# Kernel optimization log

Measured on AMD Instinct MI355X. Metric: run time of the kernel, lower is better.

Reference implementation:

```python
import jax, jax.numpy as jnp
import numpy as np

N_CLASSES = 9
N_GROUPS = 2


def setup_inputs() -> dict:
    key = jax.random.key(0)
    k1, k2 = jax.random.split(key)
    N = 16_777_216  # number of samples
    preds = jax.random.randint(k1, (N,), 0, N_CLASSES, dtype=jnp.int32)
    attrs = jax.random.randint(k2, (N,), 0, N_GROUPS, dtype=jnp.int32)
    return {"preds": preds, "attrs": attrs}


def reference(preds, attrs):
    # Fused histogram: flatten (class, group) -> single bin id in [0, 18)
    flat = preds * N_GROUPS + attrs  # [N]
    counts = jax.ops.segment_sum(
        jnp.ones_like(flat, dtype=jnp.float32), flat,
        num_segments=N_CLASSES * N_GROUPS,
    ).reshape(N_CLASSES, N_GROUPS)  # [9, 2] histogram

    n_attr_1 = jnp.sum(attrs != 0).astype(jnp.float32)
    n_attr_0 = jnp.float32(attrs.shape[0]) - n_attr_1

    diff = counts[:, 0] / n_attr_0 - counts[:, 1] / n_attr_1  # [9]
    return jnp.sum(diff * diff)
```

## Files before the change

kernel.cpp:

```cpp
#include <hip/hip_runtime.h>


#define N_CLASSES 9
#define N_GROUPS 2
#define NBINS (N_CLASSES * N_GROUPS)
#define ITEMS 4
#define BLOCK 256

typedef int v4i __attribute__((ext_vector_type(4)));

__device__ __forceinline__ void acc_item(int pv, int av,
                                         unsigned long long& acc0,
                                         unsigned long long& acc1) {
    unsigned long long inc = 1ull << (7 * pv);
    acc0 += (av == 0) ? inc : 0ull;
    acc1 += (av == 0) ? 0ull : inc;
}

__global__ __launch_bounds__(BLOCK) void spd_hist_kernel(
    const int* __restrict__ preds,
    const int* __restrict__ attrs,
    unsigned int* __restrict__ partials,
    int n4, int n)
{
    __shared__ unsigned int lh0[N_CLASSES];
    __shared__ unsigned int lh1[N_CLASSES];
    if (threadIdx.x < N_CLASSES) { lh0[threadIdx.x] = 0u; lh1[threadIdx.x] = 0u; }
    __syncthreads();

    unsigned int cnt[N_CLASSES];
    #pragma unroll
    for (int p = 0; p < N_CLASSES; ++p) cnt[p] = 0u;

    const v4i* __restrict__ p4 = (const v4i*)preds;
    const v4i* __restrict__ a4 = (const v4i*)attrs;
    const int tid = (int)threadIdx.x;

    const int span = BLOCK * ITEMS;
    const int stride = gridDim.x * span;

    v4i pb[2][ITEMS], ab[2][ITEMS];

    int S = blockIdx.x * span;
    int buf = 0;
    bool have = (S + span <= n4);

    if (have) {
        const int s = S + tid;
        #pragma unroll
        for (int k = 0; k < ITEMS; ++k) pb[0][k] = __builtin_nontemporal_load(p4 + s + k * BLOCK);
        #pragma unroll
        for (int k = 0; k < ITEMS; ++k) ab[0][k] = __builtin_nontemporal_load(a4 + s + k * BLOCK);
    }

    while (have) {
        const int Snext = S + stride;
        const bool havenext = (Snext + span <= n4);
        if (havenext) {
            const int s = Snext + tid;
            #pragma unroll
            for (int k = 0; k < ITEMS; ++k) pb[buf ^ 1][k] = __builtin_nontemporal_load(p4 + s + k * BLOCK);
            #pragma unroll
            for (int k = 0; k < ITEMS; ++k) ab[buf ^ 1][k] = __builtin_nontemporal_load(a4 + s + k * BLOCK);
        }

        unsigned long long acc0 = 0ull, acc1 = 0ull;
        #pragma unroll
        for (int k = 0; k < ITEMS; ++k) {
            acc_item(pb[buf][k].x, ab[buf][k].x, acc0, acc1);
            acc_item(pb[buf][k].y, ab[buf][k].y, acc0, acc1);
            acc_item(pb[buf][k].z, ab[buf][k].z, acc0, acc1);
            acc_item(pb[buf][k].w, ab[buf][k].w, acc0, acc1);
        }
        #pragma unroll
        for (int p = 0; p < N_CLASSES; ++p) {
            cnt[p] += ((unsigned int)(acc0 >> (7 * p)) & 127u)
                    | (((unsigned int)(acc1 >> (7 * p)) & 127u) << 16);
        }

        buf ^= 1;
        S = Snext;
        have = havenext;
    }

    if (S < n4) {
        unsigned long long acc0 = 0ull, acc1 = 0ull;
        for (int k = 0; k < ITEMS; ++k) {
            const int idx = S + tid + k * BLOCK;
            if (idx < n4) {
                v4i pp = p4[idx];
                v4i aa = a4[idx];
                acc_item(pp.x, aa.x, acc0, acc1);
                acc_item(pp.y, aa.y, acc0, acc1);
                acc_item(pp.z, aa.z, acc0, acc1);
                acc_item(pp.w, aa.w, acc0, acc1);
            }
        }
        #pragma unroll
        for (int p = 0; p < N_CLASSES; ++p) {
            cnt[p] += ((unsigned int)(acc0 >> (7 * p)) & 127u)
                    | (((unsigned int)(acc1 >> (7 * p)) & 127u) << 16);
        }
    }

    if (blockIdx.x == 0) {
        for (int t = n4 * 4 + tid; t < n; t += BLOCK)
            cnt[preds[t]] += (attrs[t] == 0) ? 1u : 0x10000u;
    }

    #pragma unroll
    for (int m = 1; m < 64; m <<= 1) {
        #pragma unroll
        for (int p = 0; p < N_CLASSES; ++p)
            cnt[p] += __shfl_xor(cnt[p], m, 64);
    }

    if ((tid & 63) == 0) {
        #pragma unroll
        for (int p = 0; p < N_CLASSES; ++p) {
            atomicAdd(&lh0[p], cnt[p] & 0xFFFFu);
            atomicAdd(&lh1[p], cnt[p] >> 16);
        }
    }
    __syncthreads();

    if (tid < NBINS) {
        int c = tid >> 1;
        unsigned int v = (tid & 1) ? lh1[c] : lh0[c];
        partials[blockIdx.x * NBINS + tid] = v;
    }
}

__global__ __launch_bounds__(1024) void spd_finalize_kernel(
    const unsigned int* __restrict__ partials,
    float* __restrict__ out, int nblocks, double n_total)
{
    __shared__ double counts[NBINS];
    const int tid = threadIdx.x;

    if (tid < NBINS * 32) {
        const int bin = tid >> 5;
        const int j = tid & 31;
        unsigned int s = 0u;
        #pragma unroll 8
        for (int b = j; b < nblocks; b += 32)
            s += partials[b * NBINS + bin];
        #pragma unroll
        for (int m = 1; m < 32; m <<= 1)
            s += __shfl_xor(s, m, 32);
        if (j == 0) counts[bin] = (double)s;
    }
    __syncthreads();

    if (tid == 0) {
        double n1 = 0.0;
        #pragma unroll
        for (int c = 0; c < N_CLASSES; ++c)
            n1 += counts[c * N_GROUPS + 1];
        double n0 = n_total - n1;
        double acc = 0.0;
        #pragma unroll
        for (int c = 0; c < N_CLASSES; ++c) {
            double d = counts[c * N_GROUPS] / n0 - counts[c * N_GROUPS + 1] / n1;
            acc += d * d;
        }
        out[0] = (float)acc;
    }
}

extern "C" void kernel_launch(void* const* d_in, const int* in_sizes, int n_in,
                              void* d_out, int out_size, void* d_ws, size_t ws_size,
                              hipStream_t stream)
{
    const int* preds = (const int*)d_in[0];
    const int* attrs = (const int*)d_in[1];
    const int n = in_sizes[0];

    unsigned int* partials = (unsigned int*)d_ws;

    const int n4 = n / 4;
    const int span = BLOCK * ITEMS;
    int grid = (n4 + span - 1) / span;
    if (grid > 1024) grid = 1024;
    int max_grid = (int)(ws_size / (NBINS * sizeof(unsigned int)));
    if (grid > max_grid) grid = max_grid;
    if (grid < 1) grid = 1;

    spd_hist_kernel<<<grid, BLOCK, 0, stream>>>(preds, attrs, partials, n4, n);
    spd_finalize_kernel<<<1, 1024, 0, stream>>>(partials, (float*)d_out, grid, (double)n);
}
```

Baseline: 157.0 us.

## Drop software double-buffering, shrink per-block work, and launch a larger grid

Removes the explicit register double-buffer prefetch loop and replaces it with a simple grid-stride loop that loads two vec4s per array per iteration. The grid cap rises from 1024 to 8192 blocks, relying on occupancy rather than manual prefetch to hide memory latency. The warp reduction now shuffles the two group counts separately instead of packed 16-bit halves, which avoids packed-lane overflow but doubles the shuffle count. The risks are more partials for the finalize kernel and possible overflow if the workspace limits the grid.

```diff
diff --git a/kernel.cpp b/kernel.cpp
--- a/kernel.cpp
+++ b/kernel.cpp
@@ -4,7 +4,7 @@
 #define N_CLASSES 9
 #define N_GROUPS 2
 #define NBINS (N_CLASSES * N_GROUPS)
-#define ITEMS 4
+#define ITEMS 2
 #define BLOCK 256
 
 typedef int v4i __attribute__((ext_vector_type(4)));
@@ -35,67 +35,35 @@
     const v4i* __restrict__ p4 = (const v4i*)preds;
     const v4i* __restrict__ a4 = (const v4i*)attrs;
     const int tid = (int)threadIdx.x;
-
     const int span = BLOCK * ITEMS;
     const int stride = gridDim.x * span;
 
-    v4i pb[2][ITEMS], ab[2][ITEMS];
+    for (int S = blockIdx.x * span; S < n4; S += stride) {
+        unsigned long long acc0 = 0ull, acc1 = 0ull;
 
-    int S = blockIdx.x * span;
-    int buf = 0;
-    bool have = (S + span <= n4);
-
-    if (have) {
-        const int s = S + tid;
-        #pragma unroll
-        for (int k = 0; k < ITEMS; ++k) pb[0][k] = __builtin_nontemporal_load(p4 + s + k * BLOCK);
-        #pragma unroll
-        for (int k = 0; k < ITEMS; ++k) ab[0][k] = __builtin_nontemporal_load(a4 + s + k * BLOCK);
-    }
-
-    while (have) {
-        const int Snext = S + stride;
-        const bool havenext = (Snext + span <= n4);
-        if (havenext) {
-            const int s = Snext + tid;
+        if (S + span <= n4) {
+            v4i p0 = __builtin_nontemporal_load(p4 + S + tid);
+            v4i p1 = __builtin_nontemporal_load(p4 + S + tid + BLOCK);
+            v4i a0 = __builtin_nontemporal_load(a4 + S + tid);
+            v4i a1 = __builtin_nontemporal_load(a4 + S + tid + BLOCK);
             #pragma unroll
-            for (int k = 0; k < ITEMS; ++k) pb[buf ^ 1][k] = __builtin_nontemporal_load(p4 + s + k * BLOCK);
-            #pragma unroll
-            for (int k = 0; k < ITEMS; ++k) ab[buf ^ 1][k] = __builtin_nontemporal_load(a4 + s + k * BLOCK);
+            for (int e = 0; e < 4; ++e) {
+                acc_item(p0[e], a0[e], acc0, acc1);
+                acc_item(p1[e], a1[e], acc0, acc1);
+            }
+        } else {
+            for (int k = 0; k < ITEMS; ++k) {
+                const int idx = S + tid + k * BLOCK;
+                if (idx < n4) {
+                    v4i pp = p4[idx];
+                    v4i aa = a4[idx];
+                    #pragma unroll
+                    for (int e = 0; e < 4; ++e)
+                        acc_item(pp[e], aa[e], acc0, acc1);
+                }
+            }
         }
 
-        unsigned long long acc0 = 0ull, acc1 = 0ull;
-        #pragma unroll
-        for (int k = 0; k < ITEMS; ++k) {
-            acc_item(pb[buf][k].x, ab[buf][k].x, acc0, acc1);
-            acc_item(pb[buf][k].y, ab[buf][k].y, acc0, acc1);
-            acc_item(pb[buf][k].z, ab[buf][k].z, acc0, acc1);
-            acc_item(pb[buf][k].w, ab[buf][k].w, acc0, acc1);
-        }
-        #pragma unroll
-        for (int p = 0; p < N_CLASSES; ++p) {
-            cnt[p] += ((unsigned int)(acc0 >> (7 * p)) & 127u)
-                    | (((unsigned int)(acc1 >> (7 * p)) & 127u) << 16);
-        }
-
-        buf ^= 1;
-        S = Snext;
-        have = havenext;
-    }
-
-    if (S < n4) {
-        unsigned long long acc0 = 0ull, acc1 = 0ull;
-        for (int k = 0; k < ITEMS; ++k) {
-            const int idx = S + tid + k * BLOCK;
-            if (idx < n4) {
-                v4i pp = p4[idx];
-                v4i aa = a4[idx];
-                acc_item(pp.x, aa.x, acc0, acc1);
-                acc_item(pp.y, aa.y, acc0, acc1);
-                acc_item(pp.z, aa.z, acc0, acc1);
-                acc_item(pp.w, aa.w, acc0, acc1);
-            }
-        }
         #pragma unroll
         for (int p = 0; p < N_CLASSES; ++p) {
             cnt[p] += ((unsigned int)(acc0 >> (7 * p)) & 127u)
@@ -108,18 +76,27 @@
             cnt[preds[t]] += (attrs[t] == 0) ? 1u : 0x10000u;
     }
 
+    unsigned int c0[N_CLASSES], c1[N_CLASSES];
+    #pragma unroll
+    for (int p = 0; p < N_CLASSES; ++p) {
+        c0[p] = cnt[p] & 0xFFFFu;
+        c1[p] = cnt[p] >> 16;
+    }
+
     #pragma unroll
     for (int m = 1; m < 64; m <<= 1) {
         #pragma unroll
-        for (int p = 0; p < N_CLASSES; ++p)
-            cnt[p] += __shfl_xor(cnt[p], m, 64);
+        for (int p = 0; p < N_CLASSES; ++p) {
+            c0[p] += __shfl_xor(c0[p], m, 64);
+            c1[p] += __shfl_xor(c1[p], m, 64);
+        }
     }
 
     if ((tid & 63) == 0) {
         #pragma unroll
         for (int p = 0; p < N_CLASSES; ++p) {
-            atomicAdd(&lh0[p], cnt[p] & 0xFFFFu);
-            atomicAdd(&lh1[p], cnt[p] >> 16);
+            atomicAdd(&lh0[p], c0[p]);
+            atomicAdd(&lh1[p], c1[p]);
         }
     }
     __syncthreads();
@@ -181,7 +158,7 @@
     const int n4 = n / 4;
     const int span = BLOCK * ITEMS;
     int grid = (n4 + span - 1) / span;
-    if (grid > 1024) grid = 1024;
+    if (grid > 8192) grid = 8192;
     int max_grid = (int)(ws_size / (NBINS * sizeof(unsigned int)));
     if (grid > max_grid) grid = max_grid;
     if (grid < 1) grid = 1;
```

After: 197.5 us. 25.8% more time.
